# Kernel optimization log

Measured on AMD Instinct MI355X. Metric: run time of the kernel, lower is better.

The kernel has to match this reference:

```python
import jax, jax.numpy as jnp
import numpy as np

B, L, F = 64, 4096, 256

def setup_inputs() -> dict:
    key = jax.random.key(0)
    x = jax.random.normal(key, (B, L, F), dtype=jnp.float32)
    return {"x": x}

def _restore(d):
    # Faithful to the torch loop (including its off-by-one):
    #   y[:, i] = cumsum(d)[:, i] for i < L-1;  y[:, L-1] = 0
    #   (the pivot add at y[:,0] is overwritten by the idx=0 iteration,
    #    and the last step is never written, staying zero)
    c = jnp.cumsum(d[:, :-1], axis=1)                      # [B, L-2, F]
    return jnp.concatenate([c, jnp.zeros_like(d[:, -1:])], axis=1)

def reference(x):
    # mode='diff'
    pivot = x[:, -1]            # stored but (due to the loop bug) never used
    d = jnp.diff(x, axis=1)     # [B, L-1, F]
    # mode='restore' on the diffed signal
    y = _restore(d)             # [B, L-1, F]
    return d, y
```

## Files before the change

kernel.cpp:

```cpp
#include <hip/hip_runtime.h>


typedef float v4f __attribute__((ext_vector_type(4)));

constexpr int B    = 64;
constexpr int L    = 4096;
constexpr int F    = 256;
constexpr int F4   = F / 4;
constexpr int LOUT = L - 1;
constexpr int ROWS = 32;

__global__ __launch_bounds__(256)
void invdiff_kernel(const float* __restrict__ x, float* __restrict__ out) {
    const int tid = threadIdx.x;
    const int f4  = tid & 63;
    const int sub = tid >> 6;
    const int b   = blockIdx.x >> 5;
    const int cb  = blockIdx.x & 31;
    const int chunk = cb * 4 + sub;
    const int r0    = chunk * ROWS;

    const v4f* xb = (const v4f*)(x + (size_t)b * L * F) + f4;
    v4f* dout = (v4f*)out + (size_t)b * LOUT * F4 + f4;
    v4f* yout = (v4f*)out + ((size_t)B * LOUT + (size_t)b * LOUT) * F4 + f4;

    const v4f x0 = xb[0];
    v4f prev = __builtin_nontemporal_load(&xb[(size_t)r0 * F4]);
    const int nrows = min(ROWS, LOUT - r0);
    const v4f zero = {0.f, 0.f, 0.f, 0.f};

    #pragma unroll 4
    for (int i = 0; i < nrows; ++i) {
        const int l = r0 + i;
        const v4f cur = __builtin_nontemporal_load(&xb[(size_t)(l + 1) * F4]);
        const v4f d  = cur - prev;
        const v4f yv = (l == LOUT - 1) ? zero : cur - x0;
        __builtin_nontemporal_store(d,  &dout[(size_t)l * F4]);
        __builtin_nontemporal_store(yv, &yout[(size_t)l * F4]);
        prev = cur;
    }
}

extern "C" void kernel_launch(void* const* d_in, const int* in_sizes, int n_in,
                              void* d_out, int out_size, void* d_ws, size_t ws_size,
                              hipStream_t stream) {
    const float* x = (const float*)d_in[0];
    float* out = (float*)d_out;
    invdiff_kernel<<<dim3(B * 32), dim3(256), 0, stream>>>(x, out);
}
```

Before: 677.0 us.

## Map one wave per output row instead of looping over row chunks

Replaces the per-thread 32-row streaming loop with a 2D grid in which each wave computes a single output row, loading both the previous and current input rows directly. This exposes far more independent memory requests and blocks to hide latency. In exchange, each input row is read twice (once as prev, once as cur), which relies on cache hits, and the nontemporal load/store hints are dropped. x0 is also reloaded by every block.

```diff
diff --git a/kernel.cpp b/kernel.cpp
--- a/kernel.cpp
+++ b/kernel.cpp
@@ -8,37 +8,26 @@
 constexpr int F    = 256;
 constexpr int F4   = F / 4;
 constexpr int LOUT = L - 1;
-constexpr int ROWS = 32;
 
 __global__ __launch_bounds__(256)
 void invdiff_kernel(const float* __restrict__ x, float* __restrict__ out) {
-    const int tid = threadIdx.x;
-    const int f4  = tid & 63;
-    const int sub = tid >> 6;
-    const int b   = blockIdx.x >> 5;
-    const int cb  = blockIdx.x & 31;
-    const int chunk = cb * 4 + sub;
-    const int r0    = chunk * ROWS;
+    const int lane = threadIdx.x & 63;
+    const int wave = threadIdx.x >> 6;
+    const int b    = blockIdx.y;
+    const int l    = blockIdx.x * 4 + wave;
+    if (l >= LOUT) return;
 
-    const v4f* xb = (const v4f*)(x + (size_t)b * L * F) + f4;
-    v4f* dout = (v4f*)out + (size_t)b * LOUT * F4 + f4;
-    v4f* yout = (v4f*)out + ((size_t)B * LOUT + (size_t)b * LOUT) * F4 + f4;
+    const v4f* xb = (const v4f*)(x + (size_t)b * L * F);
+    const v4f prev = xb[(size_t)l * F4 + lane];
+    const v4f cur  = xb[(size_t)(l + 1) * F4 + lane];
+    const v4f x0   = xb[lane];
 
-    const v4f x0 = xb[0];
-    v4f prev = __builtin_nontemporal_load(&xb[(size_t)r0 * F4]);
-    const int nrows = min(ROWS, LOUT - r0);
+    v4f* dout = (v4f*)out + ((size_t)b * LOUT + l) * F4 + lane;
+    v4f* yout = dout + (size_t)B * LOUT * F4;
+
     const v4f zero = {0.f, 0.f, 0.f, 0.f};
-
-    #pragma unroll 4
-    for (int i = 0; i < nrows; ++i) {
-        const int l = r0 + i;
-        const v4f cur = __builtin_nontemporal_load(&xb[(size_t)(l + 1) * F4]);
-        const v4f d  = cur - prev;
-        const v4f yv = (l == LOUT - 1) ? zero : cur - x0;
-        __builtin_nontemporal_store(d,  &dout[(size_t)l * F4]);
-        __builtin_nontemporal_store(yv, &yout[(size_t)l * F4]);
-        prev = cur;
-    }
+    *dout = cur - prev;
+    *yout = (l == LOUT - 1) ? zero : cur - x0;
 }
 
 extern "C" void kernel_launch(void* const* d_in, const int* in_sizes, int n_in,
@@ -46,5 +35,5 @@
                               hipStream_t stream) {
     const float* x = (const float*)d_in[0];
     float* out = (float*)d_out;
-    invdiff_kernel<<<dim3(B * 32), dim3(256), 0, stream>>>(x, out);
+    invdiff_kernel<<<dim3(1024, B), dim3(256), 0, stream>>>(x, out);
 }
```

After: 669.5 us (median of 2 runs). Within noise of the previous version (-1.1%).
